# Kernel tuning notes

Hardware: AMD Instinct MI355X
Metric: run time of the kernel (lower is better)

Reference implementation:

```python
import jax, jax.numpy as jnp
import numpy as np

B, N_PER_GRAPH = 16, 512          # uniform graphs -> to_dense_batch is a reshape
N_TOKENS = B * N_PER_GRAPH
M = 32                            # neighbors per node
D_MODEL, D_EDGE, H = 256, 128, 8


def _layernorm(x, g, b, eps=1e-5):
    m = jnp.mean(x, axis=-1, keepdims=True)
    v = jnp.mean((x - m) ** 2, axis=-1, keepdims=True)
    return (x - m) * jax.lax.rsqrt(v + eps) * g + b


def _frame_ops():
    # 2^3 = 8 sign-flip operations, matches FrameAveraging.create_ops
    d = jnp.array([-1.0, 1.0], dtype=jnp.float32)
    g = jnp.meshgrid(d, d, d, indexing='ij')
    return jnp.stack(g, axis=-1).reshape(8, 3)


def _forward(token_embs, geo_feats, edge_feats, neighbor_indices, neighbor_masks,
             ln_qkv_g, ln_qkv_b, W_qkv, b_qkv, ln_e_g, ln_e_b, W_qkv_e, b_qkv_e,
             w_attn, w_edge, W_gate, b_gate, W_fc1, b_fc1, ln_h_g, ln_h_b,
             W_fc2, b_fc2, W_fa, b_fa):
    n = token_embs.shape[0]
    d_head = D_MODEL // H
    de_head = D_EDGE // H
    # qkv transformation
    qkv = _layernorm(token_embs, ln_qkv_g, ln_qkv_b) @ W_qkv + b_qkv
    q, k, v = [a.reshape(n, H, d_head) for a in jnp.split(qkv, 3, axis=-1)]
    qkve = _layernorm(edge_feats, ln_e_g, ln_e_b) @ W_qkv_e + b_qkv_e
    qe, ve = [a.reshape(n, M, H, de_head) for a in jnp.split(qkve, 2, axis=-1)]
    gate = jax.nn.sigmoid(token_embs @ W_gate + b_gate)            # [n,1]
    # GAT-style MLP attention over gathered neighbors
    message = q[:, None] + k[neighbor_indices]                     # [n,M,H,d]
    attn = jnp.einsum('nmhd,d->nmh', message, w_attn) \
         + jnp.einsum('nmhe,e->nmh', qe, w_edge)
    attn = jnp.where(neighbor_masks[..., None], attn, -1e9)
    attn = jax.nn.softmax(jnp.transpose(attn, (0, 2, 1)), axis=-1)  # [n,H,M]
    # context aggregation
    v_n = v[neighbor_indices]                                      # [n,M,H,d]
    scalar_ctx = jnp.einsum('nhm,nmhd->nhd', attn, v_n).reshape(n, -1)
    edge_ctx = jnp.einsum('nhm,nmhd->nhd', attn, ve).reshape(n, -1)
    hcat = jnp.concatenate([scalar_ctx, edge_ctx], axis=-1)
    hmid = _layernorm(jax.nn.gelu(hcat @ W_fc1 + b_fc1, approximate=False), ln_h_g, ln_h_b)
    scalar_out = hmid @ W_fc2 + b_fc2 + token_embs
    # geometric branch with frame averaging (n_heads > 1 path)
    Xb = geo_feats.reshape(B, N_PER_GRAPH, 3)                      # dense batch, full mask
    center = Xb.mean(axis=1)                                       # [B,3]
    Xc = Xb - center[:, None]
    C = jax.lax.stop_gradient(jnp.einsum('bni,bnj->bij', Xc, Xc))  # backward=False -> detach
    _, V = jnp.linalg.eigh(C)                                      # symmetric, UPLO irrelevant
    ops = _frame_ops()
    F_ops = jax.lax.stop_gradient(ops[None, :, None, :] * V[:, None])  # [B,8,3,3]
    h_fr = jnp.einsum('bpj,boji->bopi', Xc, F_ops)                 # [B,8,N,3]
    geo_f = jnp.transpose(h_fr, (1, 0, 2, 3)).reshape(8, n, 3)     # frame-major, node order b*N+p
    geo_neigh = geo_f[:, neighbor_indices]                         # [8,n,M,3]
    geo_ctx = jnp.einsum('nhm,fnmd->fnhd', attn, geo_neigh)        # [8,n,H,3]
    agg = jax.nn.silu(jnp.einsum('fnhd,h->fnd', geo_ctx, W_fa) + b_fa)  # W_frame_agg
    geo_b = jnp.transpose(agg, (1, 0, 2)).reshape(B, N_PER_GRAPH, 8, 3)
    geo_b = jnp.transpose(geo_b, (0, 2, 1, 3))                     # [B,8,N,3]
    inv = jnp.einsum('boij,bopj->bopi', F_ops, geo_b).mean(axis=1) + center[:, None]
    geo_context = inv.reshape(n, 3)
    geo_out = geo_context * gate + geo_feats * (1.0 - gate)
    return scalar_out, geo_out


def setup_inputs() -> dict:
    key = jax.random.key(0)
    ks = jax.random.split(key, 16)
    r = lambda k, shape, s=0.02: (jax.random.normal(k, shape) * s).astype(jnp.float32)
    token_embs = jax.random.normal(ks[0], (N_TOKENS, D_MODEL), dtype=jnp.float32)
    geo_feats = jax.random.normal(ks[1], (N_TOKENS, 3), dtype=jnp.float32)
    edge_feats = jax.random.normal(ks[2], (N_TOKENS, M, D_EDGE), dtype=jnp.float32)
    base = (jnp.arange(N_TOKENS) // N_PER_GRAPH) * N_PER_GRAPH
    neighbor_indices = base[:, None] + jax.random.randint(ks[3], (N_TOKENS, M), 0, N_PER_GRAPH)
    batch_idx = jnp.arange(N_TOKENS) // N_PER_GRAPH
    neighbor_masks = jax.random.uniform(ks[4], (N_TOKENS, M)) < 0.9
    d_head, de_head = D_MODEL // H, D_EDGE // H
    return dict(
        token_embs=token_embs, geo_feats=geo_feats, edge_feats=edge_feats,
        neighbor_indices=neighbor_indices, batch_idx=batch_idx, neighbor_masks=neighbor_masks,
        ln_qkv_g=jnp.ones(D_MODEL), ln_qkv_b=jnp.zeros(D_MODEL),
        W_qkv=r(ks[5], (D_MODEL, 3 * D_MODEL)), b_qkv=jnp.zeros(3 * D_MODEL),
        ln_e_g=jnp.ones(D_EDGE), ln_e_b=jnp.zeros(D_EDGE),
        W_qkv_e=r(ks[6], (D_EDGE, 2 * D_EDGE)), b_qkv_e=jnp.zeros(2 * D_EDGE),
        w_attn=r(ks[7], (d_head,), 0.1), w_edge=r(ks[8], (de_head,), 0.1),
        W_gate=jnp.zeros((D_MODEL, 1)), b_gate=jnp.ones((1,)),   # _init_params
        W_fc1=r(ks[9], (D_MODEL + D_EDGE, D_MODEL)), b_fc1=jnp.zeros(D_MODEL),
        ln_h_g=jnp.ones(D_MODEL), ln_h_b=jnp.zeros(D_MODEL),
        W_fc2=r(ks[10], (D_MODEL, D_MODEL)), b_fc2=jnp.zeros(D_MODEL),
        W_fa=r(ks[11], (H,), 0.3), b_fa=jnp.zeros((1,)),
    )


def reference(token_embs, geo_feats, edge_feats, neighbor_indices, batch_idx, neighbor_masks,
              ln_qkv_g, ln_qkv_b, W_qkv, b_qkv, ln_e_g, ln_e_b, W_qkv_e, b_qkv_e,
              w_attn, w_edge, W_gate, b_gate, W_fc1, b_fc1, ln_h_g, ln_h_b,
              W_fc2, b_fc2, W_fa, b_fa):
    # batch_idx is uniform (arange // N_PER_GRAPH); dense batching handled by reshape
    return _forward(token_embs, geo_feats, edge_feats, neighbor_indices, neighbor_masks,
                    ln_qkv_g, ln_qkv_b, W_qkv, b_qkv, ln_e_g, ln_e_b, W_qkv_e, b_qkv_e,
                    w_attn, w_edge, W_gate, b_gate, W_fc1, b_fc1, ln_h_g, ln_h_b,
                    W_fc2, b_fc2, W_fa, b_fa)
```

## Files before the change

### kernel.cpp

```cpp
#include <hip/hip_runtime.h>
#include <hip/hip_fp16.h>
#include <math.h>

#define NTOK 8192
#define NPG  512
#define MNEI 32
#define DM   256
#define DE   128
#define NH   8

#define OFF_WQAK  65536u
#define OFF_BCAT  69632u
#define OFF_WEF   69904u
#define OFF_FLAG  70936u
#define OFF_QA    70944u
#define OFF_KA    136480u
#define OFF_GATE  202016u
#define OFF_VW    210208u
#define OFF_PROJ  2307360u
#define OFF_VMAT  2331936u
#define OFF_CEN   2332080u
#define OFF_HCAT  2332128u

#define OUT_GEO_OFF 2097152

__device__ __forceinline__ void fma4x4(const float4 a, const float4 w, float4* acc) {
    acc[0].x += a.x*w.x; acc[0].y += a.x*w.y; acc[0].z += a.x*w.z; acc[0].w += a.x*w.w;
    acc[1].x += a.y*w.x; acc[1].y += a.y*w.y; acc[1].z += a.y*w.z; acc[1].w += a.y*w.w;
    acc[2].x += a.z*w.x; acc[2].y += a.z*w.y; acc[2].z += a.z*w.z; acc[2].w += a.z*w.w;
    acc[3].x += a.w*w.x; acc[3].y += a.w*w.y; acc[3].z += a.w*w.z; acc[3].w += a.w*w.w;
}

__device__ __forceinline__ float dot4(const float4 a, const float4 b) {
    return a.x*b.x + a.y*b.y + a.z*b.z + a.w*b.w;
}

__global__ __launch_bounds__(256) void k_pre(
    const float* __restrict__ Wqkv, const float* __restrict__ bqkv,
    const float* __restrict__ Wqkve, const float* __restrict__ bqkve,
    const float* __restrict__ w_attn, const float* __restrict__ w_edge,
    const float* __restrict__ lneg, const float* __restrict__ lneb,
    const int* __restrict__ maskp, const float* __restrict__ geo,
    float* __restrict__ ws)
{
    int t = threadIdx.x;
    int b = blockIdx.x;

    if (b == 0) {
        __shared__ int sbad, sflt;
        if (t == 0) { sbad = 0; sflt = 0; }
        __syncthreads();
        int bad = 0, flt = 0;
        for (int i = 0; i < 256; i++) {
            unsigned int w = (unsigned int)maskp[i*256 + t];
            if (w > 1u) bad = 1;
            if (w == 0x3F800000u) flt = 1;
        }
        if (bad) atomicOr(&sbad, 1);
        if (flt) atomicOr(&sflt, 1);
        __syncthreads();
        if (t == 0) {
            int f = sflt ? 2 : (sbad ? 1 : 0);
            ((int*)(ws + OFF_FLAG))[0] = f;
        }
        return;
    }
    if (b == 1) {
        int h = t >> 5, l = t & 31;
        float p = 0.f;
        for (int q = 0; q < 4; q++) {
            int r = l + 32*q;
            float wef = 0.f;
            for (int e = 0; e < 16; e++) wef += Wqkve[r*256 + h*16 + e] * w_edge[e];
            p += lneb[r] * wef;
        }
        for (int m = 16; m >= 1; m >>= 1) p += __shfl_xor(p, m, 32);
        if (l == 0) {
            float s = p;
            for (int d = 0; d < 32; d++) s += bqkv[h*32 + d] * w_attn[d];
            for (int e = 0; e < 16; e++) s += bqkve[h*16 + e] * w_edge[e];
            ws[OFF_BCAT + h] = s;
        }
        if (l == 1) {
            float s = 0.f;
            for (int d = 0; d < 32; d++) s += bqkv[256 + h*32 + d] * w_attn[d];
            ws[OFF_BCAT + 8 + h] = s;
        }
        return;
    }
    if (b < 18) {
        int c = b - 2, k = t;
        int h = c & 7; int off = (c < 8) ? 0 : 256;
        float s = 0.f;
        for (int d = 0; d < 32; d++) s += Wqkv[k*768 + off + h*32 + d] * w_attn[d];
        ws[OFF_WQAK + c*256 + k] = s;
        return;
    }
    if (b < 22) {
        int i = (b - 18)*256 + t;
        int h = i >> 7, r = i & 127;
        float s = 0.f;
        for (int e = 0; e < 16; e++) s += Wqkve[r*256 + h*16 + e] * w_edge[e];
        ws[OFF_WEF + i] = s * lneg[r];
        return;
    }

    {
        __shared__ float sred[4 * 9];
        __shared__ float sres[9];
        __shared__ float sV[9];
        int g = b - 22;
        int wave = t >> 6, lane = t & 63;
        const float* gp = geo + (size_t)g * NPG * 3;

        float x0[2], y0[2], z0[2];
        float sx = 0.f, sy = 0.f, sz = 0.f;
        for (int i = 0; i < 2; i++) {
            int p = t + 256 * i;
            x0[i] = gp[p*3 + 0]; y0[i] = gp[p*3 + 1]; z0[i] = gp[p*3 + 2];
            sx += x0[i]; sy += y0[i]; sz += z0[i];
        }
        {
            float vals[3] = {sx, sy, sz};
            for (int q = 0; q < 3; q++) {
                float v = vals[q];
                for (int m = 32; m >= 1; m >>= 1) v += __shfl_xor(v, m, 64);
                if (lane == 0) sred[wave*9 + q] = v;
            }
        }
        __syncthreads();
        if (t < 3) {
            float s = 0.f;
            for (int w = 0; w < 4; w++) s += sred[w*9 + t];
            sres[t] = s * (1.0f / 512.0f);
        }
        __syncthreads();
        float cx = sres[0], cy = sres[1], cz = sres[2];

        float c6[6] = {0.f, 0.f, 0.f, 0.f, 0.f, 0.f};
        for (int i = 0; i < 2; i++) {
            float dx = x0[i] - cx, dy = y0[i] - cy, dz = z0[i] - cz;
            c6[0] += dx*dx; c6[1] += dx*dy; c6[2] += dx*dz;
            c6[3] += dy*dy; c6[4] += dy*dz; c6[5] += dz*dz;
        }
        for (int q = 0; q < 6; q++) {
            float v = c6[q];
            for (int m = 32; m >= 1; m >>= 1) v += __shfl_xor(v, m, 64);
            if (lane == 0) sred[wave*9 + q] = v;
        }
        __syncthreads();
        if (t < 6) {
            float s = 0.f;
            for (int w = 0; w < 4; w++) s += sred[w*9 + t];
            sres[t] = s;
        }
        __syncthreads();

        if (t == 0) {
            double a[3][3];
            a[0][0] = sres[0]; a[0][1] = a[1][0] = sres[1]; a[0][2] = a[2][0] = sres[2];
            a[1][1] = sres[3]; a[1][2] = a[2][1] = sres[4]; a[2][2] = sres[5];
            double v[3][3] = {{1,0,0},{0,1,0},{0,0,1}};
            const int ps[3] = {0, 0, 1}, qs[3] = {1, 2, 2};
            for (int sweep = 0; sweep < 10; sweep++) {
                for (int pi = 0; pi < 3; pi++) {
                    int p = ps[pi], q = qs[pi];
                    double apq = a[p][q];
                    if (fabs(apq) < 1e-300) continue;
                    double theta = (a[q][q] - a[p][p]) / (2.0 * apq);
                    double tt = ((theta >= 0.0) ? 1.0 : -1.0) / (fabs(theta) + sqrt(theta*theta + 1.0));
                    double c = 1.0 / sqrt(tt*tt + 1.0), s = tt * c;
                    int k = 3 - p - q;
                    double app = a[p][p], aqq = a[q][q], akp = a[k][p], akq = a[k][q];
                    a[p][p] = app - tt * apq;
                    a[q][q] = aqq + tt * apq;
                    a[p][q] = 0.0; a[q][p] = 0.0;
                    a[k][p] = c*akp - s*akq; a[p][k] = a[k][p];
                    a[k][q] = s*akp + c*akq; a[q][k] = a[k][q];
                    for (int kk = 0; kk < 3; kk++) {
                        double vp = v[kk][p], vq = v[kk][q];
                        v[kk][p] = c*vp - s*vq;
                        v[kk][q] = s*vp + c*vq;
                    }
                }
            }
            for (int r = 0; r < 3; r++)
                for (int c2 = 0; c2 < 3; c2++) {
                    float fv = (float)v[r][c2];
                    sV[r*3 + c2] = fv;
                    ws[OFF_VMAT + g*9 + r*3 + c2] = fv;
                }
            ws[OFF_CEN + g*3 + 0] = cx;
            ws[OFF_CEN + g*3 + 1] = cy;
            ws[OFF_CEN + g*3 + 2] = cz;
        }
        __syncthreads();

        for (int i = 0; i < 2; i++) {
            int p = t + 256 * i;
            float dx = x0[i] - cx, dy = y0[i] - cy, dz = z0[i] - cz;
            for (int c = 0; c < 3; c++) {
                float pr = dx * sV[0*3 + c] + dy * sV[1*3 + c] + dz * sV[2*3 + c];
                ws[OFF_PROJ + (size_t)(g*NPG + p)*3 + c] = pr;
            }
        }
    }
}

__global__ __launch_bounds__(256) void k_tokprep(
    const float* __restrict__ tok, const float* __restrict__ ln_g,
    const float* __restrict__ ln_b, const float* __restrict__ Wgate,
    const float* __restrict__ bgate, const float* __restrict__ Wqkv,
    const float* __restrict__ bqkv, float* __restrict__ ws)
{
    __shared__ __align__(16) float sln[256 * 12];
    int t = threadIdx.x;
    int tok0 = blockIdx.x * 8;

    #pragma unroll
    for (int q = 0; q < 8; q++)
        sln[t*12 + q] = tok[(size_t)(tok0 + q) * 256 + t];
    __syncthreads();

    int wave = t >> 6, lane = t & 63;
    for (int rr = 0; rr < 2; rr++) {
        int tt = wave * 2 + rr;
        float s = 0.f, gdot = 0.f;
        float xs[4];
        #pragma unroll
        for (int q = 0; q < 4; q++) {
            int k = lane + 64*q;
            float x = sln[k*12 + tt];
            xs[q] = x; s += x; gdot += x * Wgate[k];
        }
        for (int m = 32; m >= 1; m >>= 1) { s += __shfl_xor(s,m,64); gdot += __shfl_xor(gdot,m,64); }
        float mu = s * (1.0f/256.0f);
        float vs = 0.f;
        #pragma unroll
        for (int q = 0; q < 4; q++) { float d = xs[q]-mu; vs += d*d; }
        for (int m = 32; m >= 1; m >>= 1) vs += __shfl_xor(vs,m,64);
        float rinv = rsqrtf(vs*(1.0f/256.0f)+1e-5f);
        #pragma unroll
        for (int q = 0; q < 4; q++) {
            int k = lane + 64*q;
            sln[k*12 + tt] = (xs[q]-mu)*rinv*ln_g[k] + ln_b[k];
        }
        if (lane == 0) ws[OFF_GATE + tok0 + tt] = 1.0f/(1.0f+expf(-(gdot + bgate[0])));
    }
    __syncthreads();

    {
        int i = t >> 6, j = t & 63;
        const float* Wc = Wqkv + 512 + 4*j;
        float4 acc0 = make_float4(0.f,0.f,0.f,0.f);
        float4 acc1 = make_float4(0.f,0.f,0.f,0.f);
        #pragma unroll 8
        for (int k = 0; k < 256; k++) {
            float a0 = sln[k*12 + 2*i];
            float a1 = sln[k*12 + 2*i + 1];
            float4 w4 = *(const float4*)&Wc[(size_t)k*768];
            acc0.x += a0*w4.x; acc0.y += a0*w4.y; acc0.z += a0*w4.z; acc0.w += a0*w4.w;
            acc1.x += a1*w4.x; acc1.y += a1*w4.y; acc1.z += a1*w4.z; acc1.w += a1*w4.w;
        }
        float4 b4 = *(const float4*)&bqkv[512 + 4*j];
        int n0 = tok0 + 2*i;
        acc0.x += b4.x; acc0.y += b4.y; acc0.z += b4.z; acc0.w += b4.w;
        acc1.x += b4.x; acc1.y += b4.y; acc1.z += b4.z; acc1.w += b4.w;
        *(float4*)&ws[OFF_VW + (size_t)n0*256 + 4*j]     = acc0;
        *(float4*)&ws[OFF_VW + (size_t)(n0+1)*256 + 4*j] = acc1;
    }

    if (t < 128) {
        int col = t & 15, tp = t >> 4;
        const float* wq = ws + OFF_WQAK + col*256;
        float acc = 0.f;
        #pragma unroll 8
        for (int k4 = 0; k4 < 64; k4++) {
            float4 w4 = *(const float4*)&wq[4*k4];
            acc += w4.x * sln[(4*k4+0)*12 + tp]
                 + w4.y * sln[(4*k4+1)*12 + tp]
                 + w4.z * sln[(4*k4+2)*12 + tp]
                 + w4.w * sln[(4*k4+3)*12 + tp];
        }
        acc += ws[OFF_BCAT + col];
        int n = tok0 + tp;
        if (col < 8) ws[OFF_QA + n*8 + col] = acc;
        else         ws[OFF_KA + n*8 + (col - 8)] = acc;
    }
}

__global__ __launch_bounds__(256, 8) void k_attn(
    const float* __restrict__ edge, const int* __restrict__ nbr,
    const void* __restrict__ maskp,
    const float* __restrict__ lneg, const float* __restrict__ lneb,
    const float* __restrict__ bqkve, const float* __restrict__ Wqkve,
    const float* __restrict__ Wfa, const float* __restrict__ bfa,
    const float* __restrict__ geo, float* __restrict__ ws, float* __restrict__ out)
{
    __shared__ __align__(16) unsigned short seh[32 * 136];
    __shared__ __align__(16) float uSWE[8 * 132];
    __shared__ __align__(16) float sattn[8 * 36];
    __shared__ float srinv[32];
    __shared__ int   snbr[32];
    __shared__ float sg3[4];

    int t = threadIdx.x;
    int n = blockIdx.x;
    int g = n >> 9;
    int flag = ((const int*)(ws + OFF_FLAG))[0];

    int m = t >> 3, sub = t & 7;

    const float4* xp = (const float4*)(edge + (size_t)n * 4096 + m*128 + sub*16);
    float4 x0 = xp[0], x1 = xp[1], x2 = xp[2], x3 = xp[3];
    {
        int idx = t * 4;
        int h = idx >> 7, r = idx & 127;
        int s2 = r >> 4, c = r & 15;
        *(float4*)&uSWE[s2*132 + h*16 + c] = *(const float4*)&ws[OFF_WEF + idx];
    }
    if (t < 32) snbr[t] = nbr[n*32 + t];
    __syncthreads();

    {
        float s = x0.x+x0.y+x0.z+x0.w + x1.x+x1.y+x1.z+x1.w
                + x2.x+x2.y+x2.z+x2.w + x3.x+x3.y+x3.z+x3.w;
        for (int mm = 4; mm >= 1; mm >>= 1) s += __shfl_xor(s, mm, 8);
        float mu = s * (1.0f / 128.0f);
        x0.x-=mu; x0.y-=mu; x0.z-=mu; x0.w-=mu;
        x1.x-=mu; x1.y-=mu; x1.z-=mu; x1.w-=mu;
        x2.x-=mu; x2.y-=mu; x2.z-=mu; x2.w-=mu;
        x3.x-=mu; x3.y-=mu; x3.z-=mu; x3.w-=mu;
        float vs = dot4(x0,x0) + dot4(x1,x1) + dot4(x2,x2) + dot4(x3,x3);
        for (int mm = 4; mm >= 1; mm >>= 1) vs += __shfl_xor(vs, mm, 8);
        float rinv = rsqrtf(vs * (1.0f / 128.0f) + 1e-5f);

        unsigned int u[8];
        {
            __half2 hh;
            hh = __floats2half2_rn(x0.x, x0.y); u[0] = *(unsigned int*)&hh;
            hh = __floats2half2_rn(x0.z, x0.w); u[1] = *(unsigned int*)&hh;
            hh = __floats2half2_rn(x1.x, x1.y); u[2] = *(unsigned int*)&hh;
            hh = __floats2half2_rn(x1.z, x1.w); u[3] = *(unsigned int*)&hh;
            hh = __floats2half2_rn(x2.x, x2.y); u[4] = *(unsigned int*)&hh;
            hh = __floats2half2_rn(x2.z, x2.w); u[5] = *(unsigned int*)&hh;
            hh = __floats2half2_rn(x3.x, x3.y); u[6] = *(unsigned int*)&hh;
            hh = __floats2half2_rn(x3.z, x3.w); u[7] = *(unsigned int*)&hh;
        }
        uint4* sp = (uint4*)&seh[m*136 + sub*16];
        sp[0] = make_uint4(u[0], u[1], u[2], u[3]);
        sp[1] = make_uint4(u[4], u[5], u[6], u[7]);
        if (sub == 0) srinv[m] = rinv;

        float accl[8];
        const float* wb = &uSWE[sub*132];
        #pragma unroll
        for (int h = 0; h < 8; h++) {
            const float4* wp = (const float4*)(wb + h*16);
            accl[h] = dot4(x0,wp[0]) + dot4(x1,wp[1]) + dot4(x2,wp[2]) + dot4(x3,wp[3]);
        }
        #pragma unroll
        for (int st = 1; st < 8; st <<= 1) {
            #pragma unroll
            for (int h = 0; h < 8; h++) accl[h] += __shfl_xor(accl[h], st, 8);
        }
        float myacc = accl[0];
        #pragma unroll
        for (int h = 1; h < 8; h++) myacc = (sub == h) ? accl[h] : myacc;

        int mv;
        if (flag == 1)      mv = (int)((const unsigned char*)maskp)[n*32 + m];
        else if (flag == 2) mv = (((const float*)maskp)[n*32 + m] != 0.0f) ? 1 : 0;
        else                mv = ((const int*)maskp)[n*32 + m];

        float lg = myacc * rinv
                 + ws[OFF_QA + n*8 + sub]
                 + ws[OFF_KA + (size_t)snbr[m]*8 + sub];
        if (!mv) lg = -1e9f;
        sattn[sub*36 + m] = lg;
    }
    __syncthreads();

    {
        int h = t >> 5, m2 = t & 31;
        float x = sattn[h*36 + m2];
        float mx = x;
        for (int mm = 16; mm >= 1; mm >>= 1) mx = fmaxf(mx, __shfl_xor(mx, mm, 32));
        float e = expf(x - mx);
        float sum = e;
        for (int mm = 16; mm >= 1; mm >>= 1) sum += __shfl_xor(sum, mm, 32);
        sattn[h*36 + m2] = e / sum;
    }
    __syncthreads();

    float* sew = uSWE;

    int wave = t >> 6;
    if (wave == 0) {
        int c4 = t, h = c4 >> 3;
        const float* vw = ws + OFF_VW;
        float4 acc = make_float4(0.f,0.f,0.f,0.f);
        #pragma unroll 4
        for (int mi = 0; mi < 32; mi++) {
            float a = sattn[h*36 + mi];
            int row = snbr[mi];
            float4 v4 = *(const float4*)&vw[(size_t)row*256 + 4*c4];
            acc.x += a*v4.x; acc.y += a*v4.y; acc.z += a*v4.z; acc.w += a*v4.w;
        }
        *(float4*)&ws[OFF_HCAT + (size_t)n*384 + 4*c4] = acc;
    } else if (wave == 1) {
        int lm = t - 64;
        if (lm < 32) {
            float wmv = 0.f;
            #pragma unroll
            for (int h2 = 0; h2 < 8; h2++) wmv += Wfa[h2] * sattn[h2*36 + lm];
            int row = snbr[lm];
            const float* pp = ws + OFF_PROJ + (size_t)row*3;
            float q0 = wmv * pp[0], q1 = wmv * pp[1], q2 = wmv * pp[2];
            for (int st = 16; st >= 1; st >>= 1) {
                q0 += __shfl_xor(q0, st, 32);
                q1 += __shfl_xor(q1, st, 32);
                q2 += __shfl_xor(q2, st, 32);
            }
            if (lm < 3) {
                float sd = (lm == 0) ? q0 : (lm == 1) ? q1 : q2;
                float bb = bfa[0];
                float p1 = sd + bb, p2 = -sd + bb;
                float s1v = p1 / (1.0f + expf(-p1));
                float s2v = p2 / (1.0f + expf(-p2));
                sg3[lm] = 0.5f * (s1v - s2v);
            }
        }
    } else {
        int idx = t - 128;
        int rh = idx & 15, h = idx >> 4;
        float4 fA = make_float4(0.f,0.f,0.f,0.f);
        float4 fB = make_float4(0.f,0.f,0.f,0.f);
        #pragma unroll 4
        for (int mi = 0; mi < 32; mi++) {
            float a = sattn[h*36 + mi] * srinv[mi];
            uint4 v = *(const uint4*)&seh[mi*136 + rh*8];
            float2 f0 = __half22float2(*(__half2*)&v.x);
            float2 f1 = __half22float2(*(__half2*)&v.y);
            float2 f2 = __half22float2(*(__half2*)&v.z);
            float2 f3 = __half22float2(*(__half2*)&v.w);
            fA.x += a*f0.x; fA.y += a*f0.y; fA.z += a*f1.x; fA.w += a*f1.y;
            fB.x += a*f2.x; fB.y += a*f2.y; fB.z += a*f3.x; fB.w += a*f3.y;
        }
        float4 g4a = *(const float4*)&lneg[8*rh];
        float4 g4b = *(const float4*)&lneg[8*rh + 4];
        float4 b4a = *(const float4*)&lneb[8*rh];
        float4 b4b = *(const float4*)&lneb[8*rh + 4];
        float4 o1, o2;
        o1.x = g4a.x*fA.x + b4a.x; o1.y = g4a.y*fA.y + b4a.y;
        o1.z = g4a.z*fA.z + b4a.z; o1.w = g4a.w*fA.w + b4a.w;
        o2.x = g4b.x*fB.x + b4b.x; o2.y = g4b.y*fB.y + b4b.y;
        o2.z = g4b.z*fB.z + b4b.z; o2.w = g4b.w*fB.w + b4b.w;
        *(float4*)&sew[h*132 + 8*rh]     = o1;
        *(float4*)&sew[h*132 + 8*rh + 4] = o2;
    }
    __syncthreads();

    float* sec = (float*)seh;
    {
        int col4 = t & 31, rgrp = t >> 5;
        int h2 = col4 >> 2;
        const float* wqb = Wqkve + 128 + 4*col4;
        float4 accE = make_float4(0.f,0.f,0.f,0.f);
        #pragma unroll 4
        for (int ri = 0; ri < 16; ri++) {
            int r = rgrp*16 + ri;
            float sv = sew[h2*132 + r];
            float4 w4 = *(const float4*)&wqb[(size_t)r*256];
            accE.x += sv*w4.x; accE.y += sv*w4.y; accE.z += sv*w4.z; accE.w += sv*w4.w;
        }
        *(float4*)&sec[rgrp*128 + 4*col4] = accE;
    }
    __syncthreads();

    if (t < 128) {
        float ec = bqkve[128 + t];
        #pragma unroll
        for (int g2 = 0; g2 < 8; g2++) ec += sec[g2*128 + t];
        ws[OFF_HCAT + (size_t)n*384 + 256 + t] = ec;
    }
    if (t < 3) {
        const float* Vm = ws + OFF_VMAT + g*9;
        float gc = Vm[t*3+0]*sg3[0] + Vm[t*3+1]*sg3[1] + Vm[t*3+2]*sg3[2] + ws[OFF_CEN + g*3 + t];
        float gt = ws[OFF_GATE + n];
        out[OUT_GEO_OFF + (size_t)n*3 + t] = gc * gt + geo[(size_t)n*3 + t] * (1.0f - gt);
    }
}

__global__ __launch_bounds__(256) void k_mlp(
    const float* __restrict__ tok, const float* __restrict__ Wfc1,
    const float* __restrict__ bfc1, const float* __restrict__ lnhg,
    const float* __restrict__ lnhb, const float* __restrict__ Wfc2,
    const float* __restrict__ bfc2, const float* __restrict__ ws,
    float* __restrict__ out)
{
    __shared__ __align__(16) float A[384 * 12];
    __shared__ __align__(16) float R[128 * 16];
    int t = threadIdx.x;
    int tok0 = blockIdx.x * 8;
    int i2 = (t >> 6) & 1, kh = t >> 7, j = t & 63;
    const float* hc = ws + OFF_HCAT;

    #pragma unroll
    for (int q = 0; q < 12; q++) {
        int idx = q*256 + t;
        int tt = idx / 384;
        int k  = idx - tt*384;
        A[k*12 + tt] = hc[(size_t)tok0*384 + idx];
    }
    __syncthreads();

    float4 acc1[4];
    acc1[0] = acc1[1] = acc1[2] = acc1[3] = make_float4(0.f,0.f,0.f,0.f);
    {
        const float* wp = Wfc1 + 4*j;
        int kbase = kh * 192;
        #pragma unroll 8
        for (int kk = 0; kk < 192; kk++) {
            int k = kbase + kk;
            float4 a4 = *(const float4*)&A[k*12 + 4*i2];
            float4 w4 = *(const float4*)&wp[(size_t)k*256];
            fma4x4(a4, w4, acc1);
        }
    }
    if (kh == 1) {
        int rowid = t - 128;
        #pragma unroll
        for (int ti = 0; ti < 4; ti++) *(float4*)&R[rowid*16 + ti*4] = acc1[ti];
    }
    __syncthreads();

    float h[4][4];
    if (kh == 0) {
        float4 b4 = *(const float4*)&bfc1[4*j];
        #pragma unroll
        for (int ti = 0; ti < 4; ti++) {
            float4 p = *(const float4*)&R[t*16 + ti*4];
            float xv[4] = {acc1[ti].x + p.x + b4.x, acc1[ti].y + p.y + b4.y,
                           acc1[ti].z + p.z + b4.z, acc1[ti].w + p.w + b4.w};
            #pragma unroll
            for (int c = 0; c < 4; c++) {
                float x = xv[c];
                h[ti][c] = 0.5f * x * (1.0f + erff(x * 0.70710678118654752f));
            }
        }
        float s[4], qv[4];
        #pragma unroll
        for (int ti = 0; ti < 4; ti++) {
            s[ti]  = h[ti][0] + h[ti][1] + h[ti][2] + h[ti][3];
            qv[ti] = h[ti][0]*h[ti][0] + h[ti][1]*h[ti][1] + h[ti][2]*h[ti][2] + h[ti][3]*h[ti][3];
        }
        for (int m = 32; m >= 1; m >>= 1)
            #pragma unroll
            for (int ti = 0; ti < 4; ti++) {
                s[ti]  += __shfl_xor(s[ti], m, 64);
                qv[ti] += __shfl_xor(qv[ti], m, 64);
            }
        float4 g4 = *(const float4*)&lnhg[4*j];
        float4 b42 = *(const float4*)&lnhb[4*j];
        float gg[4] = {g4.x, g4.y, g4.z, g4.w};
        float bb[4] = {b42.x, b42.y, b42.z, b42.w};
        #pragma unroll
        for (int ti = 0; ti < 4; ti++) {
            float mu = s[ti] * (1.0f/256.0f);
            float var = qv[ti] * (1.0f/256.0f) - mu*mu;
            float rinv = rsqrtf(var + 1e-5f);
            #pragma unroll
            for (int c = 0; c < 4; c++) {
                float hn = (h[ti][c] - mu) * rinv * gg[c] + bb[c];
                A[(4*j + c)*12 + 4*i2 + ti] = hn;
            }
        }
    }
    __syncthreads();

    float4 acc2[4];
    acc2[0] = acc2[1] = acc2[2] = acc2[3] = make_float4(0.f,0.f,0.f,0.f);
    {
        const float* wp = Wfc2 + 4*j;
        int kbase = kh * 128;
        #pragma unroll 8
        for (int kk = 0; kk < 128; kk++) {
            int k = kbase + kk;
            float4 a4 = *(const float4*)&A[k*12 + 4*i2];
            float4 w4 = *(const float4*)&wp[(size_t)k*256];
            fma4x4(a4, w4, acc2);
        }
    }
    if (kh == 1) {
        int rowid = t - 128;
        #pragma unroll
        for (int ti = 0; ti < 4; ti++) *(float4*)&R[rowid*16 + ti*4] = acc2[ti];
    }
    __syncthreads();

    if (kh == 0) {
        float4 b4 = *(const float4*)&bfc2[4*j];
        #pragma unroll
        for (int ti = 0; ti < 4; ti++) {
            float4 p = *(const float4*)&R[t*16 + ti*4];
            size_t o = (size_t)(tok0 + 4*i2 + ti) * 256 + 4*j;
            float4 r4 = *(const float4*)&tok[o];
            float4 v;
            v.x = acc2[ti].x + p.x + b4.x + r4.x;
            v.y = acc2[ti].y + p.y + b4.y + r4.y;
            v.z = acc2[ti].z + p.z + b4.z + r4.z;
            v.w = acc2[ti].w + p.w + b4.w + r4.w;
            *(float4*)&out[o] = v;
        }
    }
}

extern "C" void kernel_launch(void* const* d_in, const int* in_sizes, int n_in,
                              void* d_out, int out_size, void* d_ws, size_t ws_size,
                              hipStream_t stream) {
    (void)in_sizes; (void)n_in; (void)out_size; (void)ws_size;
    const float* tok   = (const float*)d_in[0];
    const float* geo   = (const float*)d_in[1];
    const float* edge  = (const float*)d_in[2];
    const int*   nbr   = (const int*)d_in[3];
    const void*  maskp = d_in[5];
    const float* ln_qkv_g = (const float*)d_in[6];
    const float* ln_qkv_b = (const float*)d_in[7];
    const float* Wqkv  = (const float*)d_in[8];
    const float* bqkv  = (const float*)d_in[9];
    const float* ln_e_g = (const float*)d_in[10];
    const float* ln_e_b = (const float*)d_in[11];
    const float* Wqkve = (const float*)d_in[12];
    const float* bqkve = (const float*)d_in[13];
    const float* w_attn = (const float*)d_in[14];
    const float* w_edge = (const float*)d_in[15];
    const float* Wgate = (const float*)d_in[16];
    const float* bgate = (const float*)d_in[17];
    const float* Wfc1  = (const float*)d_in[18];
    const float* bfc1  = (const float*)d_in[19];
    const float* lnhg  = (const float*)d_in[20];
    const float* lnhb  = (const float*)d_in[21];
    const float* Wfc2  = (const float*)d_in[22];
    const float* bfc2  = (const float*)d_in[23];
    const float* Wfa   = (const float*)d_in[24];
    const float* bfa   = (const float*)d_in[25];
    float* ws  = (float*)d_ws;
    float* out = (float*)d_out;

    k_pre<<<dim3(38), dim3(256), 0, stream>>>(Wqkv, bqkv, Wqkve, bqkve, w_attn, w_edge,
                                              ln_e_g, ln_e_b, (const int*)maskp, geo, ws);
    k_tokprep<<<dim3(1024), dim3(256), 0, stream>>>(tok, ln_qkv_g, ln_qkv_b, Wgate, bgate,
                                                    Wqkv, bqkv, ws);
    k_attn<<<dim3(8192), dim3(256), 0, stream>>>(edge, nbr, maskp, ln_e_g, ln_e_b, bqkve,
                                                 Wqkve, Wfa, bfa, geo, ws, out);
    k_mlp<<<dim3(1024), dim3(256), 0, stream>>>(tok, Wfc1, bfc1, lnhg, lnhb, Wfc2, bfc2, ws, out);
}
```

Baseline: 392.2 us.

## Fold edge LayerNorm affine into value weights and drop attention-kernel barriers

```diff
diff --git a/kernel.cpp b/kernel.cpp
--- a/kernel.cpp
+++ b/kernel.cpp
@@ -9,6 +9,8 @@
 #define DE   128
 #define NH   8
 
+#define OFF_WEG   0u
+#define OFF_ECB   16384u
 #define OFF_WQAK  65536u
 #define OFF_BCAT  69632u
 #define OFF_WEF   69904u
@@ -101,7 +103,22 @@
         int h = i >> 7, r = i & 127;
         float s = 0.f;
         for (int e = 0; e < 16; e++) s += Wqkve[r*256 + h*16 + e] * w_edge[e];
-        ws[OFF_WEF + i] = s * lneg[r];
+        ws[OFF_WEF + (r >> 4)*128 + h*16 + (r & 15)] = s * lneg[r];
+        return;
+    }
+    if (b == 22) {
+        if (t < 128) {
+            float s = bqkve[128 + t];
+            for (int r = 0; r < 128; r++)
+                s += lneb[r] * Wqkve[r*256 + 128 + t];
+            ws[OFF_ECB + t] = s;
+        }
+        return;
+    }
+    if (b < 87) {
+        int i = (b - 23)*256 + t;
+        int r = i >> 7, c = i & 127;
+        ws[OFF_WEG + i] = lneg[r] * Wqkve[r*256 + 128 + c];
         return;
     }
 
@@ -109,7 +126,7 @@
         __shared__ float sred[4 * 9];
         __shared__ float sres[9];
         __shared__ float sV[9];
-        int g = b - 22;
+        int g = b - 87;
         int wave = t >> 6, lane = t & 63;
         const float* gp = geo + (size_t)g * NPG * 3;
 
@@ -292,17 +309,13 @@
 __global__ __launch_bounds__(256, 8) void k_attn(
     const float* __restrict__ edge, const int* __restrict__ nbr,
     const void* __restrict__ maskp,
-    const float* __restrict__ lneg, const float* __restrict__ lneb,
-    const float* __restrict__ bqkve, const float* __restrict__ Wqkve,
     const float* __restrict__ Wfa, const float* __restrict__ bfa,
     const float* __restrict__ geo, float* __restrict__ ws, float* __restrict__ out)
 {
     __shared__ __align__(16) unsigned short seh[32 * 136];
-    __shared__ __align__(16) float uSWE[8 * 132];
     __shared__ __align__(16) float sattn[8 * 36];
     __shared__ float srinv[32];
     __shared__ int   snbr[32];
-    __shared__ float sg3[4];
 
     int t = threadIdx.x;
     int n = blockIdx.x;
@@ -313,14 +326,14 @@
 
     const float4* xp = (const float4*)(edge + (size_t)n * 4096 + m*128 + sub*16);
     float4 x0 = xp[0], x1 = xp[1], x2 = xp[2], x3 = xp[3];
-    {
-        int idx = t * 4;
-        int h = idx >> 7, r = idx & 127;
-        int s2 = r >> 4, c = r & 15;
-        *(float4*)&uSWE[s2*132 + h*16 + c] = *(const float4*)&ws[OFF_WEF + idx];
-    }
+    int nb = nbr[n*32 + m];
+    float qa = ws[OFF_QA + n*8 + sub];
+    int mv;
+    if (flag == 1)      mv = (int)((const unsigned char*)maskp)[n*32 + m];
+    else if (flag == 2) mv = (((const float*)maskp)[n*32 + m] != 0.0f) ? 1 : 0;
+    else                mv = ((const int*)maskp)[n*32 + m];
+    float ka = ws[OFF_KA + (size_t)nb*8 + sub];
     if (t < 32) snbr[t] = nbr[n*32 + t];
-    __syncthreads();
 
     {
         float s = x0.x+x0.y+x0.z+x0.w + x1.x+x1.y+x1.z+x1.w
@@ -352,8 +365,8 @@
         sp[1] = make_uint4(u[4], u[5], u[6], u[7]);
         if (sub == 0) srinv[m] = rinv;
 
+        const float* wb = ws + OFF_WEF + sub*128;
         float accl[8];
-        const float* wb = &uSWE[sub*132];
         #pragma unroll
         for (int h = 0; h < 8; h++) {
             const float4* wp = (const float4*)(wb + h*16);
@@ -368,14 +381,7 @@
         #pragma unroll
         for (int h = 1; h < 8; h++) myacc = (sub == h) ? accl[h] : myacc;
 
-        int mv;
-        if (flag == 1)      mv = (int)((const unsigned char*)maskp)[n*32 + m];
-        else if (flag == 2) mv = (((const float*)maskp)[n*32 + m] != 0.0f) ? 1 : 0;
-        else                mv = ((const int*)maskp)[n*32 + m];
-
-        float lg = myacc * rinv
-                 + ws[OFF_QA + n*8 + sub]
-                 + ws[OFF_KA + (size_t)snbr[m]*8 + sub];
+        float lg = myacc * rinv + qa + ka;
         if (!mv) lg = -1e9f;
         sattn[sub*36 + m] = lg;
     }
@@ -392,8 +398,6 @@
         sattn[h*36 + m2] = e / sum;
     }
     __syncthreads();
-
-    float* sew = uSWE;
 
     int wave = t >> 6;
     if (wave == 0) {
@@ -423,72 +427,70 @@
                 q2 += __shfl_xor(q2, st, 32);
             }
             if (lm < 3) {
-                float sd = (lm == 0) ? q0 : (lm == 1) ? q1 : q2;
                 float bb = bfa[0];
-                float p1 = sd + bb, p2 = -sd + bb;
-                float s1v = p1 / (1.0f + expf(-p1));
-                float s2v = p2 / (1.0f + expf(-p2));
-                sg3[lm] = 0.5f * (s1v - s2v);
+                float qv[3] = {q0, q1, q2};
+                float sg[3];
+                #pragma unroll
+                for (int j = 0; j < 3; j++) {
+                    float p1 = qv[j] + bb, p2 = -qv[j] + bb;
+                    sg[j] = 0.5f * (p1/(1.0f+expf(-p1)) - p2/(1.0f+expf(-p2)));
+                }
+                const float* Vm = ws + OFF_VMAT + g*9;
+                float gc = Vm[lm*3+0]*sg[0] + Vm[lm*3+1]*sg[1] + Vm[lm*3+2]*sg[2]
+                         + ws[OFF_CEN + g*3 + lm];
+                float gt = ws[OFF_GATE + n];
+                out[OUT_GEO_OFF + (size_t)n*3 + lm] = gc * gt + geo[(size_t)n*3 + lm] * (1.0f - gt);
             }
         }
     } else {
         int idx = t - 128;
         int rh = idx & 15, h = idx >> 4;
-        float4 fA = make_float4(0.f,0.f,0.f,0.f);
-        float4 fB = make_float4(0.f,0.f,0.f,0.f);
-        #pragma unroll 4
-        for (int mi = 0; mi < 32; mi++) {
-            float a = sattn[h*36 + mi] * srinv[mi];
-            uint4 v = *(const uint4*)&seh[mi*136 + rh*8];
-            float2 f0 = __half22float2(*(__half2*)&v.x);
-            float2 f1 = __half22float2(*(__half2*)&v.y);
-            float2 f2 = __half22float2(*(__half2*)&v.z);
-            float2 f3 = __half22float2(*(__half2*)&v.w);
-            fA.x += a*f0.x; fA.y += a*f0.y; fA.z += a*f1.x; fA.w += a*f1.y;
-            fB.x += a*f2.x; fB.y += a*f2.y; fB.z += a*f3.x; fB.w += a*f3.y;
-        }
-        float4 g4a = *(const float4*)&lneg[8*rh];
-        float4 g4b = *(const float4*)&lneg[8*rh + 4];
-        float4 b4a = *(const float4*)&lneb[8*rh];
-        float4 b4b = *(const float4*)&lneb[8*rh + 4];
-        float4 o1, o2;
-        o1.x = g4a.x*fA.x + b4a.x; o1.y = g4a.y*fA.y + b4a.y;
-        o1.z = g4a.z*fA.z + b4a.z; o1.w = g4a.w*fA.w + b4a.w;
-        o2.x = g4b.x*fB.x + b4b.x; o2.y = g4b.y*fB.y + b4b.y;
-        o2.z = g4b.z*fB.z + b4b.z; o2.w = g4b.w*fB.w + b4b.w;
-        *(float4*)&sew[h*132 + 8*rh]     = o1;
-        *(float4*)&sew[h*132 + 8*rh + 4] = o2;
-    }
-    __syncthreads();
-
-    float* sec = (float*)seh;
-    {
-        int col4 = t & 31, rgrp = t >> 5;
-        int h2 = col4 >> 2;
-        const float* wqb = Wqkve + 128 + 4*col4;
-        float4 accE = make_float4(0.f,0.f,0.f,0.f);
-        #pragma unroll 4
-        for (int ri = 0; ri < 16; ri++) {
-            int r = rgrp*16 + ri;
-            float sv = sew[h2*132 + r];
-            float4 w4 = *(const float4*)&wqb[(size_t)r*256];
-            accE.x += sv*w4.x; accE.y += sv*w4.y; accE.z += sv*w4.z; accE.w += sv*w4.w;
-        }
-        *(float4*)&sec[rgrp*128 + 4*col4] = accE;
-    }
-    __syncthreads();
-
-    if (t < 128) {
-        float ec = bqkve[128 + t];
-        #pragma unroll
-        for (int g2 = 0; g2 < 8; g2++) ec += sec[g2*128 + t];
-        ws[OFF_HCAT + (size_t)n*384 + 256 + t] = ec;
-    }
-    if (t < 3) {
-        const float* Vm = ws + OFF_VMAT + g*9;
-        float gc = Vm[t*3+0]*sg3[0] + Vm[t*3+1]*sg3[1] + Vm[t*3+2]*sg3[2] + ws[OFF_CEN + g*3 + t];
-        float gt = ws[OFF_GATE + n];
-        out[OUT_GEO_OFF + (size_t)n*3 + t] = gc * gt + geo[(size_t)n*3 + t] * (1.0f - gt);
+        float f8[8];
+        {
+            float4 fA = make_float4(0.f,0.f,0.f,0.f);
+            float4 fB = make_float4(0.f,0.f,0.f,0.f);
+            #pragma unroll 4
+            for (int mi = 0; mi < 32; mi++) {
+                float a = sattn[h*36 + mi] * srinv[mi];
+                uint4 v = *(const uint4*)&seh[mi*136 + rh*8];
+                float2 f0 = __half22float2(*(__half2*)&v.x);
+                float2 f1 = __half22float2(*(__half2*)&v.y);
+                float2 f2 = __half22float2(*(__half2*)&v.z);
+                float2 f3 = __half22float2(*(__half2*)&v.w);
+                fA.x += a*f0.x; fA.y += a*f0.y; fA.z += a*f1.x; fA.w += a*f1.y;
+                fB.x += a*f2.x; fB.y += a*f2.y; fB.z += a*f3.x; fB.w += a*f3.y;
+            }
+            f8[0]=fA.x; f8[1]=fA.y; f8[2]=fA.z; f8[3]=fA.w;
+            f8[4]=fB.x; f8[5]=fB.y; f8[6]=fB.z; f8[7]=fB.w;
+        }
+        float ec[16];
+        #pragma unroll
+        for (int i = 0; i < 16; i++) ec[i] = 0.f;
+        const float* wg = ws + OFF_WEG;
+        #pragma unroll
+        for (int j = 0; j < 8; j++) {
+            float f = f8[j];
+            const float4* wr = (const float4*)&wg[(size_t)(8*rh + j)*128 + 16*h];
+            float4 w0 = wr[0], w1 = wr[1], w2 = wr[2], w3 = wr[3];
+            ec[0]  += f*w0.x; ec[1]  += f*w0.y; ec[2]  += f*w0.z; ec[3]  += f*w0.w;
+            ec[4]  += f*w1.x; ec[5]  += f*w1.y; ec[6]  += f*w1.z; ec[7]  += f*w1.w;
+            ec[8]  += f*w2.x; ec[9]  += f*w2.y; ec[10] += f*w2.z; ec[11] += f*w2.w;
+            ec[12] += f*w3.x; ec[13] += f*w3.y; ec[14] += f*w3.z; ec[15] += f*w3.w;
+        }
+        #pragma unroll
+        for (int k = 0; k < 4; k++) {
+            int d = 8 >> k;
+            bool hi = (rh & d) != 0;
+            #pragma unroll
+            for (int j = 0; j < 8; j++) {
+                if (j < d) {
+                    float lo = ec[j]     + __shfl_xor(ec[j],     d, 16);
+                    float hv = ec[j + d] + __shfl_xor(ec[j + d], d, 16);
+                    ec[j] = hi ? hv : lo;
+                }
+            }
+        }
+        ws[OFF_HCAT + (size_t)n*384 + 256 + idx] = ec[0] + ws[OFF_ECB + idx];
     }
 }
 
@@ -648,11 +650,10 @@
     float* ws  = (float*)d_ws;
     float* out = (float*)d_out;
 
-    k_pre<<<dim3(38), dim3(256), 0, stream>>>(Wqkv, bqkv, Wqkve, bqkve, w_attn, w_edge,
-                                              ln_e_g, ln_e_b, (const int*)maskp, geo, ws);
+    k_pre<<<dim3(103), dim3(256), 0, stream>>>(Wqkv, bqkv, Wqkve, bqkve, w_attn, w_edge,
+                                               ln_e_g, ln_e_b, (const int*)maskp, geo, ws);
     k_tokprep<<<dim3(1024), dim3(256), 0, stream>>>(tok, ln_qkv_g, ln_qkv_b, Wgate, bgate,
                                                     Wqkv, bqkv, ws);
-    k_attn<<<dim3(8192), dim3(256), 0, stream>>>(edge, nbr, maskp, ln_e_g, ln_e_b, bqkve,
-                                                 Wqkve, Wfa, bfa, geo, ws, out);
+    k_attn<<<dim3(8192), dim3(256), 0, stream>>>(edge, nbr, maskp, Wfa, bfa, geo, ws, out);
     k_mlp<<<dim3(1024), dim3(256), 0, stream>>>(tok, Wfc1, bfc1, lnhg, lnhb, Wfc2, bfc2, ws, out);
 }
```

Result: slower. 550.8 us (+40.5%).
